# Performance work log

Hardware: AMD Instinct MI355X
Metric: run time of the kernel (lower is better)

The kernel has to match this reference:

```python
import jax, jax.numpy as jnp
import numpy as np

DILS = (1, 2, 4, 8)
BN_EPS = 1e-5
NORM_EPS = 1e-12


def _affinity(xn, d):
    """Cosine affinity of each pixel with its 8 dilated 3x3 neighbors.
    xn: L2-normalized features [B,C,H,W]. Zero padding => out-of-bounds affinity = 0.
    Returns [B,8,H,W] with channels in unfold (row-major window) order, center removed,
    clamped at 0 (matches `affinity[affinity < 0] = 0`).
    """
    B, C, H, W = xn.shape
    p = jnp.pad(xn, ((0, 0), (0, 0), (d, d), (d, d)))
    chans = []
    for i in range(3):
        for j in range(3):
            if i == 1 and j == 1:
                continue  # skip center (index win_h*win_w//2 == 4)
            nb = p[:, :, i * d:i * d + H, j * d:j * d + W]
            chans.append(jnp.sum(nb * xn, axis=1))
    return jnp.maximum(jnp.stack(chans, axis=1), 0.0)


def _bn_relu(x, g, b):
    # BatchNorm2d in training mode (batch statistics, biased variance), then ReLU.
    m = jnp.mean(x, axis=(0, 2, 3), keepdims=True)
    v = jnp.var(x, axis=(0, 2, 3), keepdims=True)
    y = (x - m) / jnp.sqrt(v + BN_EPS)
    return jnp.maximum(y * g[None, :, None, None] + b[None, :, None, None], 0.0)


def setup_inputs() -> dict:
    key = jax.random.key(0)
    ks = jax.random.split(key, 8)
    B, C, H, W, sfc = 4, 32, 320, 640, 32
    inp = {"x": jax.random.normal(ks[0], (B, C, H, W), dtype=jnp.float32)}
    for i in range(4):
        inp[f"w{i+1}"] = jax.random.normal(ks[1 + i], (sfc, 8), dtype=jnp.float32) * 0.1
        inp[f"g{i+1}"] = jnp.ones((sfc,), dtype=jnp.float32)
        inp[f"b{i+1}"] = jnp.zeros((sfc,), dtype=jnp.float32)
    inp["w_last"] = jax.random.normal(ks[5], (sfc, 4 * sfc, 3, 3), dtype=jnp.float32) * 0.05
    inp["g_last"] = jnp.ones((sfc,), dtype=jnp.float32)
    inp["b_last"] = jnp.zeros((sfc,), dtype=jnp.float32)
    inp["w_final"] = jax.random.normal(ks[6], (sfc, sfc), dtype=jnp.float32) * 0.1
    return inp


def reference(x, w1, g1, b1, w2, g2, b2, w3, g3, b3, w4, g4, b4,
              w_last, g_last, b_last, w_final):
    # F.normalize(x, dim=1, p=2): x / max(||x||_2, eps)
    norm = jnp.sqrt(jnp.sum(x * x, axis=1, keepdims=True))
    xn = x / jnp.maximum(norm, NORM_EPS)

    branches = ((w1, g1, b1), (w2, g2, b2), (w3, g3, b3), (w4, g4, b4))
    feats = []
    for d, (w, g, b) in zip(DILS, branches):
        a = _affinity(xn, d)                       # [B,8,H,W]
        h = jnp.einsum('bchw,oc->bohw', a, w)      # 1x1 conv, no bias
        feats.append(_bn_relu(h, g, b))            # [B,sfc,H,W]

    cat = jnp.concatenate(feats, axis=1)           # [B,4*sfc,H,W]
    h = jax.lax.conv_general_dilated(
        cat, w_last, window_strides=(1, 1), padding=((1, 1), (1, 1)),
        dimension_numbers=('NCHW', 'OIHW', 'NCHW'))
    h = _bn_relu(h, g_last, b_last)
    out = jnp.einsum('bchw,oc->bohw', h, w_final)  # final 1x1 conv, no bias
    return out
```

## Files before the change

### kernel.cpp

```cpp
#include <hip/hip_runtime.h>
#include <math.h>

#define BB 4
#define CC0 32
#define HH 320
#define WW 640
#define HWp (HH*WW)
#define CHWp (CC0*HWp)
#define NCH (BB*HWp)
#define CCAT 128

#define WT_OFF  ((size_t)0)
#define ST_OFF  ((size_t)36864)
#define SC_OFF  ((size_t)37184)
#define CATF_OFF ((size_t)37504)

typedef unsigned short ushort_t;
typedef __attribute__((ext_vector_type(8)))  short    short8;
typedef __attribute__((ext_vector_type(16))) float    float16v;
typedef _Float16 h8 __attribute__((ext_vector_type(8)));
typedef _Float16 h2 __attribute__((ext_vector_type(2)));

static __device__ __forceinline__ float bf2f(ushort_t u) {
  unsigned x = ((unsigned)u) << 16;
  float f; __builtin_memcpy(&f, &x, 4); return f;
}
static __device__ __forceinline__ ushort_t f2bf(float f) {
  unsigned x; __builtin_memcpy(&x, &f, 4);
  unsigned r = (x + 0x7fffu + ((x >> 16) & 1u)) >> 16;
  return (ushort_t)r;
}
static __device__ __forceinline__ unsigned pack2(float a, float b) {
  return (unsigned)f2bf(a) | ((unsigned)f2bf(b) << 16);
}
static __device__ __forceinline__ unsigned pack2h(float a, float b) {
  h2 t; t[0] = (_Float16)a; t[1] = (_Float16)b;
  unsigned u; __builtin_memcpy(&u, &t, 4); return u;
}
static __device__ __forceinline__ void unpack8(uint4 u, float* f) {
  f[0] = bf2f((ushort_t)(u.x & 0xffff)); f[1] = bf2f((ushort_t)(u.x >> 16));
  f[2] = bf2f((ushort_t)(u.y & 0xffff)); f[3] = bf2f((ushort_t)(u.y >> 16));
  f[4] = bf2f((ushort_t)(u.z & 0xffff)); f[5] = bf2f((ushort_t)(u.z >> 16));
  f[6] = bf2f((ushort_t)(u.w & 0xffff)); f[7] = bf2f((ushort_t)(u.w >> 16));
}

__global__ __launch_bounds__(256) void k_normalize(const float* __restrict__ x,
                                                   ushort_t* __restrict__ xnh) {
  int p2 = blockIdx.x * 256 + threadIdx.x;
  int b  = blockIdx.y;
  const float2* xp = (const float2*)(x + (size_t)b * CHWp) + p2;
  float va[32], vb[32];
  float sa = 0.f, sb = 0.f;
  #pragma unroll
  for (int c = 0; c < 32; ++c) {
    float2 v = xp[c * (HWp/2)];
    va[c] = v.x; vb[c] = v.y;
    sa = fmaf(v.x, v.x, sa); sb = fmaf(v.y, v.y, sb);
  }
  float ia = 1.f / fmaxf(sqrtf(sa), 1e-12f);
  float ib = 1.f / fmaxf(sqrtf(sb), 1e-12f);
  uint4* op = (uint4*)(xnh + ((size_t)b * HWp + (size_t)p2 * 2) * 32);
  #pragma unroll
  for (int q = 0; q < 4; ++q) {
    uint4 u;
    u.x = pack2h(va[q*8+0]*ia, va[q*8+1]*ia);
    u.y = pack2h(va[q*8+2]*ia, va[q*8+3]*ia);
    u.z = pack2h(va[q*8+4]*ia, va[q*8+5]*ia);
    u.w = pack2h(va[q*8+6]*ia, va[q*8+7]*ia);
    op[q] = u;
  }
  #pragma unroll
  for (int q = 0; q < 4; ++q) {
    uint4 u;
    u.x = pack2h(vb[q*8+0]*ib, vb[q*8+1]*ib);
    u.y = pack2h(vb[q*8+2]*ib, vb[q*8+3]*ib);
    u.z = pack2h(vb[q*8+4]*ib, vb[q*8+5]*ib);
    u.w = pack2h(vb[q*8+6]*ib, vb[q*8+7]*ib);
    op[4 + q] = u;
  }
}

__global__ __launch_bounds__(256, 4) void k_branch(const ushort_t* __restrict__ xnh,
                                                   const float* __restrict__ w0,
                                                   const float* __restrict__ w1,
                                                   const float* __restrict__ w2,
                                                   const float* __restrict__ w3,
                                                   ushort_t* __restrict__ cat) {
  int z = blockIdx.z;
  int d = 1 << z;
  const float* w = (z == 0) ? w0 : (z == 1) ? w1 : (z == 2) ? w2 : w3;
  int bx = blockIdx.x;
  bx = (bx & 7) * 100 + (bx >> 3);
  int pix = bx * 256 + threadIdx.x;
  int b   = blockIdx.y;
  int y = pix / WW;
  int x = pix - y * WW;

  const ushort_t* cp0 = xnh + ((size_t)b * HWp + pix) * 32;
  h8 cen[4];
  {
    const h8* cv = (const h8*)cp0;
    #pragma unroll
    for (int q = 0; q < 4; ++q) cen[q] = cv[q];
  }

  const int DY[8] = {-1,-1,-1, 0, 0, 1, 1, 1};
  const int DX[8] = {-1, 0, 1,-1, 1,-1, 0, 1};
  float a[8];
  #pragma unroll
  for (int k = 0; k < 8; ++k) {
    int dy = DY[k] * d, dx = DX[k] * d;
    bool ok = ((unsigned)(y + dy) < (unsigned)HH) && ((unsigned)(x + dx) < (unsigned)WW);
    int ofs = ok ? (dy * WW + dx) : 0;
    const h8* np = (const h8*)(cp0 + (ptrdiff_t)ofs * 32);
    h8 n0 = np[0], n1 = np[1], n2 = np[2], n3 = np[3];
    h8 p = __builtin_elementwise_fma(cen[1], n1, cen[0] * n0);
    p = __builtin_elementwise_fma(cen[2], n2, p);
    p = __builtin_elementwise_fma(cen[3], n3, p);
    h2 t0 = __builtin_shufflevector(p, p, 0, 1);
    h2 t1 = __builtin_shufflevector(p, p, 2, 3);
    h2 t2 = __builtin_shufflevector(p, p, 4, 5);
    h2 t3 = __builtin_shufflevector(p, p, 6, 7);
    h2 t = (t0 + t1) + (t2 + t3);
    float aff = (float)t[0] + (float)t[1];
    a[k] = ok ? fmaxf(aff, 0.f) : 0.f;
  }

  uint4* cp = (uint4*)(cat + ((size_t)z * NCH + (size_t)b * HWp + pix) * 32);
  #pragma unroll
  for (int q = 0; q < 4; ++q) {
    unsigned pw[4];
    #pragma unroll
    for (int pp = 0; pp < 4; ++pp) {
      int o = q * 8 + pp * 2;
      float h0 = 0.f, h1 = 0.f;
      #pragma unroll
      for (int k = 0; k < 8; ++k) {
        h0 = fmaf(a[k], w[o * 8 + k], h0);
        h1 = fmaf(a[k], w[(o + 1) * 8 + k], h1);
      }
      pw[pp] = pack2(h0, h1);
    }
    uint4 u; u.x = pw[0]; u.y = pw[1]; u.z = pw[2]; u.w = pw[3];
    cp[q] = u;
  }
}

__global__ __launch_bounds__(256) void k_stats_cat(const ushort_t* __restrict__ cat,
                                                   float* __restrict__ g_s,
                                                   float* __restrict__ g_q) {
  int t  = threadIdx.x;
  int cg = t & 3;
  int pr = t >> 2;
  int blk = blockIdx.x;
  int z = blk / 400;
  size_t row0 = (size_t)blk * 2048 + pr;
  const uint4* base = (const uint4*)cat;
  float s[8] = {0,0,0,0,0,0,0,0}, q[8] = {0,0,0,0,0,0,0,0};
  for (int j = 0; j < 32; ++j) {
    uint4 u = base[(row0 + (size_t)j * 64) * 4 + cg];
    float v[8]; unpack8(u, v);
    #pragma unroll
    for (int i = 0; i < 8; ++i) { s[i] += v[i]; q[i] = fmaf(v[i], v[i], q[i]); }
  }
  __shared__ float ls[64][32], lq[64][32];
  #pragma unroll
  for (int i = 0; i < 8; ++i) { ls[pr][cg*8+i] = s[i]; lq[pr][cg*8+i] = q[i]; }
  __syncthreads();
  if (t < 32) {
    float a = 0.f, bq = 0.f;
    for (int r = 0; r < 64; ++r) { a += ls[r][t]; bq += lq[r][t]; }
    atomicAdd(g_s + z * 32 + t, a); atomicAdd(g_q + z * 32 + t, bq);
  }
}

__global__ __launch_bounds__(256) void k_stats_f32(const float* __restrict__ t,
                                                   float* __restrict__ g_s,
                                                   float* __restrict__ g_q) {
  int c = blockIdx.y, b = blockIdx.z;
  size_t base = ((size_t)b * 32 + c) * HWp + (size_t)blockIdx.x * 8192;
  const float4* p = (const float4*)(t + base) + threadIdx.x;
  float s = 0.f, q = 0.f;
  #pragma unroll
  for (int j = 0; j < 8; ++j) {
    float4 v = p[j * 256];
    s += v.x + v.y + v.z + v.w;
    q = fmaf(v.x, v.x, q); q = fmaf(v.y, v.y, q);
    q = fmaf(v.z, v.z, q); q = fmaf(v.w, v.w, q);
  }
  #pragma unroll
  for (int off = 32; off > 0; off >>= 1) {
    s += __shfl_down(s, off, 64);
    q += __shfl_down(q, off, 64);
  }
  __shared__ float ls[4], lq[4];
  int lane = threadIdx.x & 63, wid = threadIdx.x >> 6;
  if (lane == 0) { ls[wid] = s; lq[wid] = q; }
  __syncthreads();
  if (threadIdx.x == 0) {
    float ts = 0, tq = 0;
    #pragma unroll
    for (int i = 0; i < 4; ++i) { ts += ls[i]; tq += lq[i]; }
    atomicAdd(g_s + c, ts); atomicAdd(g_q + c, tq);
  }
}

__global__ void k_bnfin(const float* __restrict__ s, const float* __restrict__ q,
                        const float* g0, const float* g1, const float* g2, const float* g3,
                        const float* b0, const float* b1, const float* b2, const float* b3,
                        float* __restrict__ scale, float* __restrict__ shift, int Cc) {
  int c = threadIdx.x;
  if (c >= Cc) return;
  const float* g; const float* bb; int ci;
  if (Cc == 128) {
    int z = c >> 5; ci = c & 31;
    g  = (z == 0) ? g0 : (z == 1) ? g1 : (z == 2) ? g2 : g3;
    bb = (z == 0) ? b0 : (z == 1) ? b1 : (z == 2) ? b2 : b3;
  } else { g = g0; bb = b0; ci = c; }
  float mean = s[c] / (float)NCH;
  float var  = q[c] / (float)NCH - mean * mean;
  float inv  = 1.f / sqrtf(var + 1e-5f);
  float scv  = g[ci] * inv;
  scale[c] = scv;
  shift[c] = bb[ci] - mean * scv;
}

__global__ void k_wt(const float* __restrict__ wl, ushort_t* __restrict__ wbf) {
  int idx = blockIdx.x * 256 + threadIdx.x;
  if (idx >= 9 * 8 * 64 * 8) return;
  int j = idx & 7;
  int l = (idx >> 3) & 63;
  int tc = idx >> 9;
  int t = tc >> 3, cg = tc & 7;
  int o = l & 31;
  int ch = cg * 16 + ((l >> 5) << 3) + j;
  wbf[idx] = f2bf(wl[(o * 128 + ch) * 9 + t]);
}

#define SROWS 6
#define SCOLS 34
#define CHPAD 72
__global__ __launch_bounds__(256, 4) void k_conv(const ushort_t* __restrict__ cat,
                                                 const ushort_t* __restrict__ wbf,
                                                 const float* __restrict__ scale,
                                                 const float* __restrict__ shift,
                                                 float* __restrict__ out) {
  __shared__ __align__(16) ushort_t s_in[SROWS * SCOLS * CHPAD];
  int lane = threadIdx.x;
  int w    = threadIdx.y;
  int tid  = w * 64 + lane;
  int gx0 = blockIdx.x * 32, gy0 = blockIdx.y * 4;
  int b = blockIdx.z;
  size_t bHW = (size_t)b * HWp;

  const short8* wfr = (const short8*)wbf;
  float16v acc = {};

  int site0 = tid >> 3;
  int chp   = tid & 7;

  #pragma unroll
  for (int r = 0; r < 2; ++r) {
    int chb = r * 64 + chp * 8;
    int zp  = chb >> 5;
    int chi = chb & 31;
    const ushort_t* catz = cat + (size_t)zp * ((size_t)NCH * 32);
    float4 sc0 = *(const float4*)&scale[chb];
    float4 sc1 = *(const float4*)&scale[chb + 4];
    float4 sh0 = *(const float4*)&shift[chb];
    float4 sh1 = *(const float4*)&shift[chb + 4];
    float scl[8] = {sc0.x,sc0.y,sc0.z,sc0.w,sc1.x,sc1.y,sc1.z,sc1.w};
    float shf[8] = {sh0.x,sh0.y,sh0.z,sh0.w,sh1.x,sh1.y,sh1.z,sh1.w};

    if (r) __syncthreads();
    for (int s = site0; s < SROWS * SCOLS; s += 32) {
      int row = s / SCOLS, col = s - row * SCOLS;
      int gy = gy0 - 1 + row, gx = gx0 - 1 + col;
      uint4 u = {0u,0u,0u,0u};
      if ((unsigned)gy < (unsigned)HH && (unsigned)gx < (unsigned)WW) {
        uint4 raw = *(const uint4*)&catz[(bHW + (size_t)gy * WW + gx) * 32 + chi];
        unsigned rw[4] = {raw.x, raw.y, raw.z, raw.w};
        unsigned pk[4];
        #pragma unroll
        for (int q = 0; q < 4; ++q) {
          float v0 = fmaxf(fmaf(bf2f((ushort_t)(rw[q] & 0xffff)), scl[q*2],   shf[q*2]),   0.f);
          float v1 = fmaxf(fmaf(bf2f((ushort_t)(rw[q] >> 16)),    scl[q*2+1], shf[q*2+1]), 0.f);
          pk[q] = pack2(v0, v1);
        }
        u.x = pk[0]; u.y = pk[1]; u.z = pk[2]; u.w = pk[3];
      }
      *(uint4*)&s_in[(size_t)s * CHPAD + chp * 8] = u;
    }
    __syncthreads();

    int pcol = lane & 31;
    int half = lane >> 5;
    #pragma unroll
    for (int t = 0; t < 9; ++t) {
      int ky = t / 3, kx = t - ky * 3;
      int rowbase = ((w + ky) * SCOLS + pcol + kx) * CHPAD + half * 8;
      #pragma unroll
      for (int c = 0; c < 4; ++c) {
        short8 bfrag = wfr[(t * 8 + r * 4 + c) * 64 + lane];
        short8 afrag = *(const short8*)&s_in[rowbase + c * 16];
        acc = __builtin_amdgcn_mfma_f32_32x32x16_bf16(afrag, bfrag, acc, 0, 0, 0);
      }
    }
  }

  __syncthreads();
  float* epi = (float*)s_in + w * (32 * 33);
  int half = lane >> 5, mm = lane & 31;
  #pragma unroll
  for (int r16 = 0; r16 < 16; ++r16) {
    int m = (r16 & 3) + 8 * (r16 >> 2) + 4 * half;
    epi[m * 33 + mm] = acc[r16];
  }
  __syncthreads();
  size_t obase = bHW + (size_t)(gy0 + w) * WW + gx0 + mm;
  #pragma unroll
  for (int i = 0; i < 16; ++i) {
    int o = half * 16 + i;
    out[(size_t)o * HWp + obase + (size_t)b * (CHWp - HWp)] = epi[mm * 33 + o];
  }
}

__global__ __launch_bounds__(256) void k_final(const float* hin,
                                               const float* __restrict__ wf,
                                               const float* __restrict__ scale,
                                               const float* __restrict__ shift,
                                               float* out) {
  int p2 = blockIdx.x * 256 + threadIdx.x;
  int b  = blockIdx.y;
  const float2* hp = (const float2*)(hin + (size_t)b * CHWp) + p2;
  float va[32], vb[32];
  #pragma unroll
  for (int c = 0; c < 32; ++c) {
    float2 v = hp[c * (HWp/2)];
    va[c] = fmaxf(fmaf(v.x, scale[c], shift[c]), 0.f);
    vb[c] = fmaxf(fmaf(v.y, scale[c], shift[c]), 0.f);
  }
  float2* op = (float2*)(out + (size_t)b * CHWp) + p2;
  #pragma unroll
  for (int o = 0; o < 32; ++o) {
    float ra = 0.f, rb = 0.f;
    #pragma unroll
    for (int c = 0; c < 32; ++c) {
      float wv = wf[o * 32 + c];
      ra = fmaf(va[c], wv, ra);
      rb = fmaf(vb[c], wv, rb);
    }
    float2 rr; rr.x = ra; rr.y = rb;
    op[o * (HWp/2)] = rr;
  }
}

extern "C" void kernel_launch(void* const* d_in, const int* in_sizes, int n_in,
                              void* d_out, int out_size, void* d_ws, size_t ws_size,
                              hipStream_t stream) {
  const float* x      = (const float*)d_in[0];
  const float* w1     = (const float*)d_in[1];
  const float* g1     = (const float*)d_in[2];
  const float* b1     = (const float*)d_in[3];
  const float* w2     = (const float*)d_in[4];
  const float* g2     = (const float*)d_in[5];
  const float* b2     = (const float*)d_in[6];
  const float* w3     = (const float*)d_in[7];
  const float* g3     = (const float*)d_in[8];
  const float* b3     = (const float*)d_in[9];
  const float* w4     = (const float*)d_in[10];
  const float* g4     = (const float*)d_in[11];
  const float* b4     = (const float*)d_in[12];
  const float* w_last = (const float*)d_in[13];
  const float* g_last = (const float*)d_in[14];
  const float* b_last = (const float*)d_in[15];
  const float* w_fin  = (const float*)d_in[16];

  float* ws = (float*)d_ws;
  ushort_t* wbf = (ushort_t*)(ws + WT_OFF);
  float*    st  = ws + ST_OFF;
  float*    sc  = ws + SC_OFF;
  ushort_t* cat = (ushort_t*)(ws + CATF_OFF);

  ushort_t* xnh = (ushort_t*)d_out;
  float*    xn  = (float*)d_out;

  hipMemsetAsync(st, 0, 320 * sizeof(float), stream);

  k_normalize<<<dim3(400, 4), 256, 0, stream>>>(x, xnh);
  k_branch<<<dim3(800, 4, 4), 256, 0, stream>>>(xnh, w1, w2, w3, w4, cat);
  k_stats_cat<<<1600, 256, 0, stream>>>(cat, st, st + 128);
  k_bnfin<<<1, 128, 0, stream>>>(st, st + 128, g1, g2, g3, g4, b1, b2, b3, b4,
                                 sc, sc + 128, 128);
  k_wt<<<144, 256, 0, stream>>>(w_last, wbf);
  k_conv<<<dim3(20, 80, 4), dim3(64, 4), 0, stream>>>(cat, wbf, sc, sc + 128, xn);
  k_stats_f32<<<dim3(25, 32, 4), 256, 0, stream>>>(xn, st + 256, st + 288);
  k_bnfin<<<1, 128, 0, stream>>>(st + 256, st + 288, g_last, g_last, g_last, g_last,
                                 b_last, b_last, b_last, b_last, sc + 256, sc + 288, 32);
  k_final<<<dim3(400, 4), 256, 0, stream>>>(xn, w_fin, sc + 256, sc + 288, (float*)d_out);
}
```

Baseline: 580.8 us.

## Fuse branch BN statistics into affinity kernel with quad-lane channel split

```diff
diff --git a/kernel.cpp b/kernel.cpp
--- a/kernel.cpp
+++ b/kernel.cpp
@@ -80,97 +80,98 @@
   }
 }
 
-__global__ __launch_bounds__(256, 4) void k_branch(const ushort_t* __restrict__ xnh,
-                                                   const float* __restrict__ w0,
-                                                   const float* __restrict__ w1,
-                                                   const float* __restrict__ w2,
-                                                   const float* __restrict__ w3,
-                                                   ushort_t* __restrict__ cat) {
+__global__ __launch_bounds__(256, 4) void k_branch2(const ushort_t* __restrict__ xnh,
+                                                    const float* __restrict__ w0,
+                                                    const float* __restrict__ w1,
+                                                    const float* __restrict__ w2,
+                                                    const float* __restrict__ w3,
+                                                    ushort_t* __restrict__ cat,
+                                                    float* __restrict__ g_s,
+                                                    float* __restrict__ g_q) {
   int z = blockIdx.z;
   int d = 1 << z;
   const float* w = (z == 0) ? w0 : (z == 1) ? w1 : (z == 2) ? w2 : w3;
   int bx = blockIdx.x;
   bx = (bx & 7) * 100 + (bx >> 3);
-  int pix = bx * 256 + threadIdx.x;
-  int b   = blockIdx.y;
-  int y = pix / WW;
-  int x = pix - y * WW;
-
-  const ushort_t* cp0 = xnh + ((size_t)b * HWp + pix) * 32;
-  h8 cen[4];
-  {
-    const h8* cv = (const h8*)cp0;
-    #pragma unroll
-    for (int q = 0; q < 4; ++q) cen[q] = cv[q];
-  }
+  int tid   = threadIdx.x;
+  int laneq = tid & 3;
+  int prow  = tid >> 2;
+  int b = blockIdx.y;
+
+  const ushort_t* xb = xnh + (size_t)b * HWp * 32 + laneq * 8;
+  ushort_t* cb = cat + ((size_t)z * NCH + (size_t)b * HWp) * 32 + laneq * 8;
 
   const int DY[8] = {-1,-1,-1, 0, 0, 1, 1, 1};
   const int DX[8] = {-1, 0, 1,-1, 1,-1, 0, 1};
-  float a[8];
-  #pragma unroll
-  for (int k = 0; k < 8; ++k) {
-    int dy = DY[k] * d, dx = DX[k] * d;
-    bool ok = ((unsigned)(y + dy) < (unsigned)HH) && ((unsigned)(x + dx) < (unsigned)WW);
-    int ofs = ok ? (dy * WW + dx) : 0;
-    const h8* np = (const h8*)(cp0 + (ptrdiff_t)ofs * 32);
-    h8 n0 = np[0], n1 = np[1], n2 = np[2], n3 = np[3];
-    h8 p = __builtin_elementwise_fma(cen[1], n1, cen[0] * n0);
-    p = __builtin_elementwise_fma(cen[2], n2, p);
-    p = __builtin_elementwise_fma(cen[3], n3, p);
-    h2 t0 = __builtin_shufflevector(p, p, 0, 1);
-    h2 t1 = __builtin_shufflevector(p, p, 2, 3);
-    h2 t2 = __builtin_shufflevector(p, p, 4, 5);
-    h2 t3 = __builtin_shufflevector(p, p, 6, 7);
-    h2 t = (t0 + t1) + (t2 + t3);
-    float aff = (float)t[0] + (float)t[1];
-    a[k] = ok ? fmaxf(aff, 0.f) : 0.f;
-  }
-
-  uint4* cp = (uint4*)(cat + ((size_t)z * NCH + (size_t)b * HWp + pix) * 32);
-  #pragma unroll
-  for (int q = 0; q < 4; ++q) {
-    unsigned pw[4];
-    #pragma unroll
-    for (int pp = 0; pp < 4; ++pp) {
-      int o = q * 8 + pp * 2;
-      float h0 = 0.f, h1 = 0.f;
+
+  float sv[8] = {0,0,0,0,0,0,0,0}, qv[8] = {0,0,0,0,0,0,0,0};
+
+  #pragma unroll 1
+  for (int it = 0; it < 4; ++it) {
+    int pix = bx * 256 + it * 64 + prow;
+    int y = pix / WW;
+    int x = pix - y * WW;
+    const ushort_t* cp0 = xb + (size_t)pix * 32;
+    h8 cen = *(const h8*)cp0;
+
+    float a[8];
+    #pragma unroll
+    for (int k = 0; k < 8; ++k) {
+      int dy = DY[k] * d, dx = DX[k] * d;
+      bool ok = ((unsigned)(y + dy) < (unsigned)HH) && ((unsigned)(x + dx) < (unsigned)WW);
+      int ofs = ok ? (dy * WW + dx) : 0;
+      h8 n = *(const h8*)(cp0 + (ptrdiff_t)ofs * 32);
+      h8 p = cen * n;
+      h2 s01 = __builtin_shufflevector(p, p, 0, 1) + __builtin_shufflevector(p, p, 2, 3);
+      h2 s23 = __builtin_shufflevector(p, p, 4, 5) + __builtin_shufflevector(p, p, 6, 7);
+      h2 sh = s01 + s23;
+      float part = (float)sh[0] + (float)sh[1];
+      part += __shfl_xor(part, 1, 64);
+      part += __shfl_xor(part, 2, 64);
+      a[k] = ok ? fmaxf(part, 0.f) : 0.f;
+    }
+
+    float r[8];
+    #pragma unroll
+    for (int j = 0; j < 8; ++j) {
+      int o = laneq * 8 + j;
+      float h = 0.f;
       #pragma unroll
-      for (int k = 0; k < 8; ++k) {
-        h0 = fmaf(a[k], w[o * 8 + k], h0);
-        h1 = fmaf(a[k], w[(o + 1) * 8 + k], h1);
-      }
-      pw[pp] = pack2(h0, h1);
-    }
-    uint4 u; u.x = pw[0]; u.y = pw[1]; u.z = pw[2]; u.w = pw[3];
-    cp[q] = u;
-  }
-}
-
-__global__ __launch_bounds__(256) void k_stats_cat(const ushort_t* __restrict__ cat,
-                                                   float* __restrict__ g_s,
-                                                   float* __restrict__ g_q) {
-  int t  = threadIdx.x;
-  int cg = t & 3;
-  int pr = t >> 2;
-  int blk = blockIdx.x;
-  int z = blk / 400;
-  size_t row0 = (size_t)blk * 2048 + pr;
-  const uint4* base = (const uint4*)cat;
-  float s[8] = {0,0,0,0,0,0,0,0}, q[8] = {0,0,0,0,0,0,0,0};
-  for (int j = 0; j < 32; ++j) {
-    uint4 u = base[(row0 + (size_t)j * 64) * 4 + cg];
-    float v[8]; unpack8(u, v);
-    #pragma unroll
-    for (int i = 0; i < 8; ++i) { s[i] += v[i]; q[i] = fmaf(v[i], v[i], q[i]); }
-  }
-  __shared__ float ls[64][32], lq[64][32];
-  #pragma unroll
-  for (int i = 0; i < 8; ++i) { ls[pr][cg*8+i] = s[i]; lq[pr][cg*8+i] = q[i]; }
+      for (int k = 0; k < 8; ++k) h = fmaf(a[k], w[o * 8 + k], h);
+      r[j] = h;
+      sv[j] += h;
+      qv[j] = fmaf(h, h, qv[j]);
+    }
+    uint4 u;
+    u.x = pack2(r[0], r[1]); u.y = pack2(r[2], r[3]);
+    u.z = pack2(r[4], r[5]); u.w = pack2(r[6], r[7]);
+    *(uint4*)(cb + (size_t)pix * 32) = u;
+  }
+
+  #pragma unroll
+  for (int off = 4; off < 64; off <<= 1) {
+    #pragma unroll
+    for (int j = 0; j < 8; ++j) {
+      sv[j] += __shfl_down(sv[j], off, 64);
+      qv[j] += __shfl_down(qv[j], off, 64);
+    }
+  }
+  __shared__ float lsum[4][4][16];
+  int wid = tid >> 6, lane = tid & 63;
+  if (lane < 4) {
+    #pragma unroll
+    for (int j = 0; j < 8; ++j) {
+      lsum[wid][lane][j]     = sv[j];
+      lsum[wid][lane][8 + j] = qv[j];
+    }
+  }
   __syncthreads();
-  if (t < 32) {
-    float a = 0.f, bq = 0.f;
-    for (int r = 0; r < 64; ++r) { a += ls[r][t]; bq += lq[r][t]; }
-    atomicAdd(g_s + z * 32 + t, a); atomicAdd(g_q + z * 32 + t, bq);
+  if (tid < 64) {
+    int lq = tid >> 4, sl = tid & 15;
+    float t = lsum[0][lq][sl] + lsum[1][lq][sl] + lsum[2][lq][sl] + lsum[3][lq][sl];
+    int ch = z * 32 + lq * 8 + (sl & 7);
+    if (sl < 8) atomicAdd(g_s + ch, t);
+    else        atomicAdd(g_q + ch, t);
   }
 }
 
@@ -388,8 +389,8 @@
   hipMemsetAsync(st, 0, 320 * sizeof(float), stream);
 
   k_normalize<<<dim3(400, 4), 256, 0, stream>>>(x, xnh);
-  k_branch<<<dim3(800, 4, 4), 256, 0, stream>>>(xnh, w1, w2, w3, w4, cat);
-  k_stats_cat<<<1600, 256, 0, stream>>>(cat, st, st + 128);
+  k_branch2<<<dim3(800, 4, 4), 256, 0, stream>>>(xnh, w1, w2, w3, w4, cat,
+                                                 st, st + 128);
   k_bnfin<<<1, 128, 0, stream>>>(st, st + 128, g1, g2, g3, g4, b1, b2, b3, b4,
                                  sc, sc + 128, 128);
   k_wt<<<144, 256, 0, stream>>>(w_last, wbf);
```

Result: slower. 604.6 us (+4.1%).

## Fuse BN statistics into branch and conv kernels, stage neighbor loads in LDS

Applied to the files above, without the earlier changes.

```diff
diff --git a/kernel.cpp b/kernel.cpp
--- a/kernel.cpp
+++ b/kernel.cpp
@@ -9,6 +9,7 @@
 #define CHWp (CC0*HWp)
 #define NCH (BB*HWp)
 #define CCAT 128
+#define BBHW ((long)BB*HWp)
 
 #define WT_OFF  ((size_t)0)
 #define ST_OFF  ((size_t)36864)
@@ -36,12 +37,6 @@
 static __device__ __forceinline__ unsigned pack2h(float a, float b) {
   h2 t; t[0] = (_Float16)a; t[1] = (_Float16)b;
   unsigned u; __builtin_memcpy(&u, &t, 4); return u;
-}
-static __device__ __forceinline__ void unpack8(uint4 u, float* f) {
-  f[0] = bf2f((ushort_t)(u.x & 0xffff)); f[1] = bf2f((ushort_t)(u.x >> 16));
-  f[2] = bf2f((ushort_t)(u.y & 0xffff)); f[3] = bf2f((ushort_t)(u.y >> 16));
-  f[4] = bf2f((ushort_t)(u.z & 0xffff)); f[5] = bf2f((ushort_t)(u.z >> 16));
-  f[6] = bf2f((ushort_t)(u.w & 0xffff)); f[7] = bf2f((ushort_t)(u.w >> 16));
 }
 
 __global__ __launch_bounds__(256) void k_normalize(const float* __restrict__ x,
@@ -80,53 +75,86 @@
   }
 }
 
-__global__ __launch_bounds__(256, 4) void k_branch(const ushort_t* __restrict__ xnh,
-                                                   const float* __restrict__ w0,
-                                                   const float* __restrict__ w1,
-                                                   const float* __restrict__ w2,
-                                                   const float* __restrict__ w3,
-                                                   ushort_t* __restrict__ cat) {
+__global__ __launch_bounds__(256, 4) void k_branch3(const ushort_t* __restrict__ xnh,
+                                                    const float* __restrict__ w0,
+                                                    const float* __restrict__ w1,
+                                                    const float* __restrict__ w2,
+                                                    const float* __restrict__ w3,
+                                                    ushort_t* __restrict__ cat,
+                                                    float* __restrict__ g_s,
+                                                    float* __restrict__ g_q) {
+  __shared__ __align__(16) ushort_t sbuf[256 * 40];
+  __shared__ float part[16][16][4];
+
   int z = blockIdx.z;
   int d = 1 << z;
   const float* w = (z == 0) ? w0 : (z == 1) ? w1 : (z == 2) ? w2 : w3;
   int bx = blockIdx.x;
   bx = (bx & 7) * 100 + (bx >> 3);
-  int pix = bx * 256 + threadIdx.x;
-  int b   = blockIdx.y;
+  int tid = threadIdx.x;
+  int b = blockIdx.y;
+  int pix0 = bx * 256;
+  int pix = pix0 + tid;
   int y = pix / WW;
   int x = pix - y * WW;
 
-  const ushort_t* cp0 = xnh + ((size_t)b * HWp + pix) * 32;
-  h8 cen[4];
-  {
-    const h8* cv = (const h8*)cp0;
-    #pragma unroll
-    for (int q = 0; q < 4; ++q) cen[q] = cv[q];
-  }
-
   const int DY[8] = {-1,-1,-1, 0, 0, 1, 1, 1};
   const int DX[8] = {-1, 0, 1,-1, 1,-1, 0, 1};
+
+  h8 cen0, cen1, cen2, cen3;
   float a[8];
-  #pragma unroll
-  for (int k = 0; k < 8; ++k) {
-    int dy = DY[k] * d, dx = DX[k] * d;
-    bool ok = ((unsigned)(y + dy) < (unsigned)HH) && ((unsigned)(x + dx) < (unsigned)WW);
-    int ofs = ok ? (dy * WW + dx) : 0;
-    const h8* np = (const h8*)(cp0 + (ptrdiff_t)ofs * 32);
-    h8 n0 = np[0], n1 = np[1], n2 = np[2], n3 = np[3];
-    h8 p = __builtin_elementwise_fma(cen[1], n1, cen[0] * n0);
-    p = __builtin_elementwise_fma(cen[2], n2, p);
-    p = __builtin_elementwise_fma(cen[3], n3, p);
-    h2 t0 = __builtin_shufflevector(p, p, 0, 1);
-    h2 t1 = __builtin_shufflevector(p, p, 2, 3);
-    h2 t2 = __builtin_shufflevector(p, p, 4, 5);
-    h2 t3 = __builtin_shufflevector(p, p, 6, 7);
-    h2 t = (t0 + t1) + (t2 + t3);
-    float aff = (float)t[0] + (float)t[1];
-    a[k] = ok ? fmaxf(aff, 0.f) : 0.f;
-  }
-
-  uint4* cp = (uint4*)(cat + ((size_t)z * NCH + (size_t)b * HWp + pix) * 32);
+
+  #pragma unroll
+  for (int wv = 0; wv < 9; ++wv) {
+    int dy = wv ? DY[wv-1] * d : 0;
+    int dx = wv ? DX[wv-1] * d : 0;
+    long g = (long)b * HWp + pix0 + dy * WW + dx;
+
+    __syncthreads();
+    if (g >= 0 && g <= BBHW - 256) {
+      const ushort_t* src = xnh + g * 32;
+      #pragma unroll
+      for (int q = 0; q < 4; ++q) {
+        uint4 v = *(const uint4*)(src + q * 2048 + tid * 8);
+        int slot = q * 64 + (tid >> 2), j = tid & 3;
+        *(uint4*)(sbuf + slot * 40 + j * 8) = v;
+      }
+    } else {
+      #pragma unroll
+      for (int q = 0; q < 4; ++q) {
+        long uo = g * 32 + q * 2048 + tid * 8;
+        long hi = BBHW * 32 - 8;
+        uo = uo < 0 ? 0 : (uo > hi ? hi : uo);
+        uint4 v = *(const uint4*)(xnh + uo);
+        int slot = q * 64 + (tid >> 2), j = tid & 3;
+        *(uint4*)(sbuf + slot * 40 + j * 8) = v;
+      }
+    }
+    __syncthreads();
+
+    const ushort_t* sl = sbuf + tid * 40;
+    h8 n0 = *(const h8*)(sl);
+    h8 n1 = *(const h8*)(sl + 8);
+    h8 n2 = *(const h8*)(sl + 16);
+    h8 n3 = *(const h8*)(sl + 24);
+    if (wv == 0) {
+      cen0 = n0; cen1 = n1; cen2 = n2; cen3 = n3;
+    } else {
+      int k = wv - 1;
+      bool ok = ((unsigned)(y + dy) < (unsigned)HH) && ((unsigned)(x + dx) < (unsigned)WW);
+      h8 p = __builtin_elementwise_fma(cen1, n1, cen0 * n0);
+      p = __builtin_elementwise_fma(cen2, n2, p);
+      p = __builtin_elementwise_fma(cen3, n3, p);
+      h2 s01 = __builtin_shufflevector(p, p, 0, 1) + __builtin_shufflevector(p, p, 2, 3);
+      h2 s23 = __builtin_shufflevector(p, p, 4, 5) + __builtin_shufflevector(p, p, 6, 7);
+      h2 sh = s01 + s23;
+      float aff = (float)sh[0] + (float)sh[1];
+      a[k] = ok ? fmaxf(aff, 0.f) : 0.f;
+    }
+  }
+
+  ushort_t* cb = cat + ((size_t)z * NCH + (size_t)b * HWp + pix) * 32;
+  uint4* cslot = (uint4*)(sbuf + tid * 40);
   #pragma unroll
   for (int q = 0; q < 4; ++q) {
     unsigned pw[4];
@@ -142,66 +170,33 @@
       pw[pp] = pack2(h0, h1);
     }
     uint4 u; u.x = pw[0]; u.y = pw[1]; u.z = pw[2]; u.w = pw[3];
-    cp[q] = u;
-  }
-}
-
-__global__ __launch_bounds__(256) void k_stats_cat(const ushort_t* __restrict__ cat,
-                                                   float* __restrict__ g_s,
-                                                   float* __restrict__ g_q) {
-  int t  = threadIdx.x;
-  int cg = t & 3;
-  int pr = t >> 2;
-  int blk = blockIdx.x;
-  int z = blk / 400;
-  size_t row0 = (size_t)blk * 2048 + pr;
-  const uint4* base = (const uint4*)cat;
-  float s[8] = {0,0,0,0,0,0,0,0}, q[8] = {0,0,0,0,0,0,0,0};
-  for (int j = 0; j < 32; ++j) {
-    uint4 u = base[(row0 + (size_t)j * 64) * 4 + cg];
-    float v[8]; unpack8(u, v);
-    #pragma unroll
-    for (int i = 0; i < 8; ++i) { s[i] += v[i]; q[i] = fmaf(v[i], v[i], q[i]); }
-  }
-  __shared__ float ls[64][32], lq[64][32];
-  #pragma unroll
-  for (int i = 0; i < 8; ++i) { ls[pr][cg*8+i] = s[i]; lq[pr][cg*8+i] = q[i]; }
+    ((uint4*)cb)[q] = u;
+    cslot[q] = u;
+  }
   __syncthreads();
-  if (t < 32) {
-    float a = 0.f, bq = 0.f;
-    for (int r = 0; r < 64; ++r) { a += ls[r][t]; bq += lq[r][t]; }
-    atomicAdd(g_s + z * 32 + t, a); atomicAdd(g_q + z * 32 + t, bq);
-  }
-}
-
-__global__ __launch_bounds__(256) void k_stats_f32(const float* __restrict__ t,
-                                                   float* __restrict__ g_s,
-                                                   float* __restrict__ g_q) {
-  int c = blockIdx.y, b = blockIdx.z;
-  size_t base = ((size_t)b * 32 + c) * HWp + (size_t)blockIdx.x * 8192;
-  const float4* p = (const float4*)(t + base) + threadIdx.x;
-  float s = 0.f, q = 0.f;
-  #pragma unroll
-  for (int j = 0; j < 8; ++j) {
-    float4 v = p[j * 256];
-    s += v.x + v.y + v.z + v.w;
-    q = fmaf(v.x, v.x, q); q = fmaf(v.y, v.y, q);
-    q = fmaf(v.z, v.z, q); q = fmaf(v.w, v.w, q);
-  }
-  #pragma unroll
-  for (int off = 32; off > 0; off >>= 1) {
-    s += __shfl_down(s, off, 64);
-    q += __shfl_down(q, off, 64);
-  }
-  __shared__ float ls[4], lq[4];
-  int lane = threadIdx.x & 63, wid = threadIdx.x >> 6;
-  if (lane == 0) { ls[wid] = s; lq[wid] = q; }
+
+  {
+    int grp = tid >> 4, c2 = tid & 15;
+    float s0 = 0.f, q0 = 0.f, s1 = 0.f, q1 = 0.f;
+    #pragma unroll
+    for (int p2i = 0; p2i < 16; ++p2i) {
+      unsigned uu = *(const unsigned*)(sbuf + (grp * 16 + p2i) * 40 + c2 * 2);
+      float v0 = bf2f((ushort_t)(uu & 0xffff));
+      float v1 = bf2f((ushort_t)(uu >> 16));
+      s0 += v0; q0 = fmaf(v0, v0, q0);
+      s1 += v1; q1 = fmaf(v1, v1, q1);
+    }
+    part[grp][c2][0] = s0; part[grp][c2][1] = q0;
+    part[grp][c2][2] = s1; part[grp][c2][3] = q1;
+  }
   __syncthreads();
-  if (threadIdx.x == 0) {
-    float ts = 0, tq = 0;
-    #pragma unroll
-    for (int i = 0; i < 4; ++i) { ts += ls[i]; tq += lq[i]; }
-    atomicAdd(g_s + c, ts); atomicAdd(g_q + c, tq);
+  if (tid < 64) {
+    int cc = tid >> 2, v = tid & 3;
+    float t = 0.f;
+    #pragma unroll
+    for (int gg = 0; gg < 16; ++gg) t += part[gg][cc][v];
+    int ch = z * 32 + cc * 2 + (v >> 1);
+    atomicAdd(((v & 1) == 0 ? g_s : g_q) + ch, t);
   }
 }
 
@@ -244,8 +239,11 @@
                                                  const ushort_t* __restrict__ wbf,
                                                  const float* __restrict__ scale,
                                                  const float* __restrict__ shift,
-                                                 float* __restrict__ out) {
+                                                 float* __restrict__ out,
+                                                 float* __restrict__ g_s2,
+                                                 float* __restrict__ g_q2) {
   __shared__ __align__(16) ushort_t s_in[SROWS * SCOLS * CHPAD];
+  __shared__ float cstat[4][32][2];
   int lane = threadIdx.x;
   int w    = threadIdx.y;
   int tid  = w * 64 + lane;
@@ -308,7 +306,21 @@
     }
   }
 
+  {
+    float s2 = 0.f, q2 = 0.f;
+    #pragma unroll
+    for (int r16 = 0; r16 < 16; ++r16) { float v = acc[r16]; s2 += v; q2 = fmaf(v, v, q2); }
+    s2 += __shfl_down(s2, 32, 64);
+    q2 += __shfl_down(q2, 32, 64);
+    if (lane < 32) { cstat[w][lane][0] = s2; cstat[w][lane][1] = q2; }
+  }
+
   __syncthreads();
+  if (tid < 64) {
+    int ch = tid & 31, v = tid >> 5;
+    float t4 = cstat[0][ch][v] + cstat[1][ch][v] + cstat[2][ch][v] + cstat[3][ch][v];
+    atomicAdd((v == 0 ? g_s2 : g_q2) + ch, t4);
+  }
   float* epi = (float*)s_in + w * (32 * 33);
   int half = lane >> 5, mm = lane & 31;
   #pragma unroll
@@ -388,13 +400,13 @@
   hipMemsetAsync(st, 0, 320 * sizeof(float), stream);
 
   k_normalize<<<dim3(400, 4), 256, 0, stream>>>(x, xnh);
-  k_branch<<<dim3(800, 4, 4), 256, 0, stream>>>(xnh, w1, w2, w3, w4, cat);
-  k_stats_cat<<<1600, 256, 0, stream>>>(cat, st, st + 128);
+  k_branch3<<<dim3(800, 4, 4), 256, 0, stream>>>(xnh, w1, w2, w3, w4, cat,
+                                                 st, st + 128);
   k_bnfin<<<1, 128, 0, stream>>>(st, st + 128, g1, g2, g3, g4, b1, b2, b3, b4,
                                  sc, sc + 128, 128);
   k_wt<<<144, 256, 0, stream>>>(w_last, wbf);
-  k_conv<<<dim3(20, 80, 4), dim3(64, 4), 0, stream>>>(cat, wbf, sc, sc + 128, xn);
-  k_stats_f32<<<dim3(25, 32, 4), 256, 0, stream>>>(xn, st + 256, st + 288);
+  k_conv<<<dim3(20, 80, 4), dim3(64, 4), 0, stream>>>(cat, wbf, sc, sc + 128, xn,
+                                                      st + 256, st + 288);
   k_bnfin<<<1, 128, 0, stream>>>(st + 256, st + 288, g_last, g_last, g_last, g_last,
                                  b_last, b_last, b_last, b_last, sc + 256, sc + 288, 32);
   k_final<<<dim3(400, 4), 256, 0, stream>>>(xn, w_fin, sc + 256, sc + 288, (float*)d_out);
```

New measurement: 628.9 us. +8.3%, slower.
